# Performance work log

Measured on AMD Instinct MI355X. Metric: run time of the kernel, lower is better.

## Reference

```python
import jax, jax.numpy as jnp
import numpy as np

EPS = 1e-8      # F.normalize eps in _cos_angle
TOPK = 4
DELTA = 1.0     # huber delta
EXTRA_FRAMES = (1, 3, 5, 7)            # teacher-only frames
SHARED = ((2, 1), (4, 2), (6, 3))      # (teacher_idx, student_idx) for shared frames


def _huber(e):
    ae = jnp.abs(e)
    return jnp.where(ae <= DELTA, 0.5 * e * e, DELTA * (ae - 0.5 * DELTA))


def _angles(R, H, Sh):
    # R: [b,r,d] ref, H: [b,r,k,d] sim_high, Sh: [b,s,d] shared.
    # Cosines of the three triplet angles computed via dot-product expansion,
    # avoiding any [b,r,s,k,d] intermediate. cos = (u.v)/(max(|u|,eps)*max(|v|,eps))
    RH  = jnp.einsum('brd,brkd->brk', R, H)
    RSh = jnp.einsum('brd,bsd->brs', R, Sh)
    HSh = jnp.einsum('brkd,bsd->brsk', H, Sh)
    Rn2  = jnp.sum(R * R, -1)        # [b,r]
    Hn2  = jnp.sum(H * H, -1)        # [b,r,k]
    Shn2 = jnp.sum(Sh * Sh, -1)      # [b,s]
    n_RSh = jnp.maximum(jnp.sqrt(jnp.maximum(Rn2[:, :, None] + Shn2[:, None, :] - 2 * RSh, 0.0)), EPS)          # |R-Sh| [b,r,s]
    n_RH  = jnp.maximum(jnp.sqrt(jnp.maximum(Rn2[:, :, None] + Hn2 - 2 * RH, 0.0)), EPS)                        # |R-H|  [b,r,k]
    n_HSh = jnp.maximum(jnp.sqrt(jnp.maximum(Hn2[:, :, None, :] + Shn2[:, None, :, None] - 2 * HSh, 0.0)), EPS) # |H-Sh| [b,r,s,k]
    # angle1: vertex=ref, u=Sh-R, v=H-R
    d1 = HSh - RSh[..., None] - RH[:, :, None, :] + Rn2[:, :, None, None]
    a1 = d1 / (n_RSh[..., None] * n_RH[:, :, None, :])
    # angle2: vertex=H, u=R-H, v=Sh-H
    d2 = RSh[..., None] - RH[:, :, None, :] - HSh + Hn2[:, :, None, :]
    a2 = d2 / (n_RH[:, :, None, :] * n_HSh)
    # angle3: vertex=Sh, u=R-Sh, v=H-Sh
    d3 = RH[:, :, None, :] - RSh[..., None] - HSh + Shn2[:, None, :, None]
    a3 = d3 / (n_RSh[..., None] * n_HSh)
    return a1, a2, a3


def setup_inputs() -> dict:
    key = jax.random.key(0)
    k1, k2, k3, k4 = jax.random.split(key, 4)
    B, S_T, P, D = 2, 8, 2048, 1024
    num_ref, num_shared = 128, 128
    teacher_feats = jax.random.normal(k1, (B, S_T, P, D), jnp.float32)
    student_feats = jax.random.normal(k2, (B, 4, P, D), jnp.float32)
    ref_perm = jax.random.permutation(k3, P)[:num_ref].astype(jnp.int32)
    shared_perm = jax.random.permutation(k4, P)[:num_shared].astype(jnp.int32)
    return {"teacher_feats": teacher_feats, "student_feats": student_feats,
            "ref_perm": ref_perm, "shared_perm": shared_perm}


def reference(teacher_feats, student_feats, ref_perm, shared_perm):
    tf = jax.lax.stop_gradient(teacher_feats)  # teacher is fully detached
    B, _, P, D = tf.shape
    num_ref = ref_perm.shape[0]
    num_shared = shared_perm.shape[0]
    ref_t = tf[:, 0, ref_perm, :]                 # [B,R,D]
    ref_s = student_feats[:, 0, ref_perm, :]
    # teacher-only frames, concatenated along patch dim -> [B, EP, D]
    extra = tf[:, jnp.array(EXTRA_FRAMES), :, :].reshape(B, -1, D)
    # cosine-similarity retrieval (selection_mode='topk')
    rtn = ref_t / jnp.maximum(jnp.linalg.norm(ref_t, axis=-1, keepdims=True), 1e-12)
    etn = extra / jnp.maximum(jnp.linalg.norm(extra, axis=-1, keepdims=True), 1e-12)
    sim = jnp.einsum('brd,bed->bre', rtn, etn)
    _, idx = jax.lax.top_k(sim, TOPK)             # [B,R,K]
    H = jnp.take_along_axis(extra, idx.reshape(B, -1, 1), axis=1).reshape(B, num_ref, TOPK, D)
    s1 = s2 = s3 = jnp.float32(0.0)
    for tidx, sidx in SHARED:
        Sh_t = tf[:, tidx, shared_perm, :]
        Sh_s = student_feats[:, sidx, shared_perm, :]
        a1t, a2t, a3t = _angles(ref_t, H, Sh_t)
        a1s, a2s, a3s = _angles(ref_s, H, Sh_s)
        s1 = s1 + _huber(a1s - a1t).sum()
        s2 = s2 + _huber(a2s - a2t).sum()
        s3 = s3 + _huber(a3s - a3t).sum()
    total = jnp.float32(len(SHARED) * B * num_ref * num_shared * TOPK)
    # angle weights all 1.0
    loss = s1 / total + s2 / total + s3 / total
    return loss
```

## Files before the change

kernel.cpp:

```cpp
#include <hip/hip_runtime.h>
#include <cstdint>
#include <cstddef>
#include <cfloat>
#include <climits>

#define D_DIM   1024
#define P_DIM   2048
#define NB      2
#define NR      128
#define NS      128
#define KTOP    4
#define E_DIM   8192
#define ANG_EPS 1e-8f
#define M_PAIR  768
#define N_PAIR  768

#define SIM_SLICES  4
#define SIM_KSLICE  256
#define PAIR_SLICES 8
#define PAIR_KSLICE 128

#define TOPK_DELTA  0.25f
#define MAXCAND     128
#define LOSS_BLOCKS (NR * NB * 3)

typedef short short8 __attribute__((ext_vector_type(8)));
typedef float f32x4 __attribute__((ext_vector_type(4)));

__device__ __forceinline__ float dot4(float4 a, float4 b) {
  return a.x * b.x + a.y * b.y + a.z * b.z + a.w * b.w;
}

__device__ __forceinline__ float huber(float e) {
  float ae = fabsf(e);
  return ae <= 1.0f ? 0.5f * e * e : ae - 0.5f;
}

__device__ __forceinline__ bool better(float va, int ia, float vb, int ib) {
  return (va > vb) || (va == vb && ia < ib);
}

__device__ __forceinline__ unsigned int f2bf(float x) {
  union { float f; unsigned int u; } v; v.f = x;
  unsigned int r = v.u + 0x7fffu + ((v.u >> 16) & 1u);
  return r >> 16;
}
__device__ __forceinline__ unsigned int pk2bf(float x, float y) {
  return f2bf(x) | (f2bf(y) << 16);
}

__device__ __forceinline__ float block_reduce_sum(float v, float* scratch) {
  #pragma unroll
  for (int o = 32; o > 0; o >>= 1) v += __shfl_down(v, o);
  __syncthreads();
  if ((threadIdx.x & 63) == 0) scratch[threadIdx.x >> 6] = v;
  __syncthreads();
  float r = 0.0f;
  int nw = (int)(blockDim.x >> 6);
  if ((int)threadIdx.x < nw) r = scratch[threadIdx.x];
  #pragma unroll
  for (int o = 2; o > 0; o >>= 1) r += __shfl_down(r, o);
  return r;
}

__global__ __launch_bounds__(256) void sim_gemm_kernel(const float* __restrict__ tf,
                                                       const int* __restrict__ ref_perm,
                                                       float* __restrict__ simP,
                                                       float* __restrict__ bn2P) {
  __shared__ unsigned int Ah[128 * 20];
  __shared__ unsigned int Bh[128 * 20];
  __shared__ const float* Arow[128];
  __shared__ const float* Brow[128];
  const int tid = threadIdx.x;
  const int b = blockIdx.z;
  const int slice = blockIdx.y;
  const int nbase = blockIdx.x * 128;
  const int kbase = slice * SIM_KSLICE;
  if (tid < 128) {
    Arow[tid] = tf + ((size_t)(b * 8) * P_DIM + ref_perm[tid]) * D_DIM + kbase;
  } else {
    int n = nbase + (tid - 128);
    Brow[tid - 128] = tf + ((size_t)(b * 8 + 1 + 2 * (n >> 11)) * P_DIM + (n & (P_DIM - 1))) * D_DIM + kbase;
  }
  __syncthreads();

  const int srow = tid >> 1;
  const int shalf = (tid & 1) * 16;
  const float* asrc = Arow[srow] + shalf;
  const float* bsrc = Brow[srow] + shalf;

  float4 av[4], bv[4];
  #pragma unroll
  for (int i = 0; i < 4; ++i) {
    av[i] = *(const float4*)(asrc + 4 * i);
    bv[i] = *(const float4*)(bsrc + 4 * i);
  }

  const int wave = tid >> 6;
  const int lane = tid & 63;
  const int fr = lane & 15;
  const int q16 = (lane >> 4) * 16;
  const char* Ab = (const char*)Ah;
  const char* Bb = (const char*)Bh;

  f32x4 acc[2][8];
  #pragma unroll
  for (int mt = 0; mt < 2; ++mt)
    #pragma unroll
    for (int nt = 0; nt < 8; ++nt)
      #pragma unroll
      for (int r = 0; r < 4; ++r) acc[mt][nt][r] = 0.0f;

  float bn2 = 0.0f;
  unsigned int* adst = Ah + srow * 20 + (tid & 1) * 8;
  unsigned int* bdst = Bh + srow * 20 + (tid & 1) * 8;

  for (int ck = 0; ck < 8; ++ck) {
    bn2 += dot4(bv[0], bv[0]) + dot4(bv[1], bv[1]) + dot4(bv[2], bv[2]) + dot4(bv[3], bv[3]);
    unsigned int ua[8], ub[8];
    #pragma unroll
    for (int i = 0; i < 4; ++i) {
      ua[2 * i]     = pk2bf(av[i].x, av[i].y);
      ua[2 * i + 1] = pk2bf(av[i].z, av[i].w);
      ub[2 * i]     = pk2bf(bv[i].x, bv[i].y);
      ub[2 * i + 1] = pk2bf(bv[i].z, bv[i].w);
    }
    __syncthreads();
    *(uint4*)(adst)     = make_uint4(ua[0], ua[1], ua[2], ua[3]);
    *(uint4*)(adst + 4) = make_uint4(ua[4], ua[5], ua[6], ua[7]);
    *(uint4*)(bdst)     = make_uint4(ub[0], ub[1], ub[2], ub[3]);
    *(uint4*)(bdst + 4) = make_uint4(ub[4], ub[5], ub[6], ub[7]);
    __syncthreads();
    if (ck < 7) {
      const float* an = asrc + (ck + 1) * 32;
      const float* bn = bsrc + (ck + 1) * 32;
      #pragma unroll
      for (int i = 0; i < 4; ++i) {
        av[i] = *(const float4*)(an + 4 * i);
        bv[i] = *(const float4*)(bn + 4 * i);
      }
    }
    short8 afr[2], bfr[8];
    #pragma unroll
    for (int mt = 0; mt < 2; ++mt)
      afr[mt] = *(const short8*)(Ab + (wave * 32 + mt * 16 + fr) * 80 + q16);
    #pragma unroll
    for (int nt = 0; nt < 8; ++nt)
      bfr[nt] = *(const short8*)(Bb + (nt * 16 + fr) * 80 + q16);
    #pragma unroll
    for (int mt = 0; mt < 2; ++mt)
      #pragma unroll
      for (int nt = 0; nt < 8; ++nt)
        acc[mt][nt] = __builtin_amdgcn_mfma_f32_16x16x32_bf16(afr[mt], bfr[nt], acc[mt][nt], 0, 0, 0);
  }

  bn2 += __shfl_xor(bn2, 1);
  if ((tid & 1) == 0)
    bn2P[((size_t)slice * NB + b) * E_DIM + nbase + srow] = bn2;

  float* base = simP + (((size_t)slice * NB + b) * NR) * E_DIM + nbase;
  const int crow = (lane >> 4) * 4;
  #pragma unroll
  for (int mt = 0; mt < 2; ++mt) {
    #pragma unroll
    for (int nt = 0; nt < 8; ++nt) {
      int col = nt * 16 + fr;
      #pragma unroll
      for (int r = 0; r < 4; ++r) {
        int m = wave * 32 + mt * 16 + crow + r;
        base[(size_t)m * E_DIM + col] = acc[mt][nt][r];
      }
    }
  }
}

__global__ __launch_bounds__(256) void topk_kernel(const float* __restrict__ simP,
                                                   const float* __restrict__ bn2P,
                                                   const float* __restrict__ tf,
                                                   const float* __restrict__ sf,
                                                   const int* __restrict__ ref_perm,
                                                   int* __restrict__ tki,
                                                   float* __restrict__ rt_n2,
                                                   float* __restrict__ rs_n2,
                                                   float* __restrict__ hn2,
                                                   float* __restrict__ rh_t,
                                                   float* __restrict__ rh_s) {
  __shared__ float scores[E_DIM];
  __shared__ float sv[1024];
  __shared__ int si[1024];
  __shared__ float candVal[MAXCAND];
  __shared__ int candIdx[MAXCAND];
  __shared__ int cnt;
  __shared__ int fin4[4];
  const int tid = threadIdx.x;
  const int br = blockIdx.x;
  const int b = br >> 7;
  const int r = br & 127;
  const size_t ST = (size_t)NB * NR * E_DIM;
  const size_t SN = (size_t)NB * E_DIM;
  const float* p = simP + (size_t)br * E_DIM;
  const float* q = bn2P + (size_t)b * E_DIM;
  if (tid == 0) cnt = 0;

  float tv[4] = {-FLT_MAX, -FLT_MAX, -FLT_MAX, -FLT_MAX};
  int ti[4] = {INT_MAX, INT_MAX, INT_MAX, INT_MAX};
  for (int e4 = tid * 4; e4 < E_DIM; e4 += 1024) {
    float4 s = *(const float4*)(p + e4);
    float4 s1 = *(const float4*)(p + ST + e4);
    float4 s2 = *(const float4*)(p + 2 * ST + e4);
    float4 s3 = *(const float4*)(p + 3 * ST + e4);
    float4 n0 = *(const float4*)(q + e4);
    float4 n1 = *(const float4*)(q + SN + e4);
    float4 n2 = *(const float4*)(q + 2 * SN + e4);
    float4 n3 = *(const float4*)(q + 3 * SN + e4);
    float sj[4] = {s.x + s1.x + s2.x + s3.x, s.y + s1.y + s2.y + s3.y,
                   s.z + s1.z + s2.z + s3.z, s.w + s1.w + s2.w + s3.w};
    float nj[4] = {n0.x + n1.x + n2.x + n3.x, n0.y + n1.y + n2.y + n3.y,
                   n0.z + n1.z + n2.z + n3.z, n0.w + n1.w + n2.w + n3.w};
    #pragma unroll
    for (int j = 0; j < 4; ++j) {
      int e = e4 + j;
      float x = sj[j] * rsqrtf(fmaxf(nj[j], 1e-24f));
      scores[e] = x;
      if (better(x, e, tv[3], ti[3])) {
        tv[3] = x; ti[3] = e;
        #pragma unroll
        for (int k = 3; k > 0; --k) {
          if (better(tv[k], ti[k], tv[k - 1], ti[k - 1])) {
            float fv = tv[k]; tv[k] = tv[k - 1]; tv[k - 1] = fv;
            int fi2 = ti[k]; ti[k] = ti[k - 1]; ti[k - 1] = fi2;
          }
        }
      }
    }
  }
  #pragma unroll
  for (int k = 0; k < 4; ++k) { sv[tid * 4 + k] = tv[k]; si[tid * 4 + k] = ti[k]; }
  for (int stride = 128; stride > 0; stride >>= 1) {
    __syncthreads();
    if (tid < stride) {
      float av[4], bv2[4]; int ai[4], bi2[4];
      #pragma unroll
      for (int k = 0; k < 4; ++k) {
        av[k] = sv[tid * 4 + k];               ai[k] = si[tid * 4 + k];
        bv2[k] = sv[(tid + stride) * 4 + k];   bi2[k] = si[(tid + stride) * 4 + k];
      }
      float ov[4]; int oi[4]; int pa = 0, pb = 0;
      #pragma unroll
      for (int k = 0; k < 4; ++k) {
        bool takeA = (pa < 4) && (pb >= 4 || better(av[pa], ai[pa], bv2[pb], bi2[pb]));
        if (takeA) { ov[k] = av[pa]; oi[k] = ai[pa]; ++pa; }
        else       { ov[k] = bv2[pb]; oi[k] = bi2[pb]; ++pb; }
      }
      #pragma unroll
      for (int k = 0; k < 4; ++k) { sv[tid * 4 + k] = ov[k]; si[tid * 4 + k] = oi[k]; }
    }
  }
  __syncthreads();
  const float tau = sv[3] - TOPK_DELTA;

  for (int e4 = tid * 4; e4 < E_DIM; e4 += 1024) {
    #pragma unroll
    for (int j = 0; j < 4; ++j) {
      int e = e4 + j;
      if (scores[e] >= tau) {
        int pos = atomicAdd(&cnt, 1);
        if (pos < MAXCAND) candIdx[pos] = e;
      }
    }
  }
  __syncthreads();
  int cntc = min(cnt, MAXCAND);

  const float* R = tf + ((size_t)(b * 8) * P_DIM + ref_perm[r]) * D_DIM;
  const int wave = tid >> 6;
  const int lane = tid & 63;
  for (int c = wave; c < cntc; c += 4) {
    int e = candIdx[c];
    const float* E = tf + ((size_t)(b * 8 + 1 + 2 * (e >> 11)) * P_DIM + (e & (P_DIM - 1))) * D_DIM;
    float d = 0.0f, n2 = 0.0f;
    #pragma unroll
    for (int i = 0; i < 4; ++i) {
      float4 rv = *(const float4*)(R + lane * 16 + i * 4);
      float4 ev = *(const float4*)(E + lane * 16 + i * 4);
      d += dot4(rv, ev);
      n2 += dot4(ev, ev);
    }
    #pragma unroll
    for (int o = 32; o > 0; o >>= 1) { d += __shfl_xor(d, o); n2 += __shfl_xor(n2, o); }
    if (lane == 0) candVal[c] = d / fmaxf(sqrtf(n2), 1e-12f);
  }
  __syncthreads();
  if (tid == 0) {
    float bv[4] = {-FLT_MAX, -FLT_MAX, -FLT_MAX, -FLT_MAX};
    int bi[4] = {INT_MAX, INT_MAX, INT_MAX, INT_MAX};
    for (int c = 0; c < cntc; ++c) {
      float x = candVal[c]; int e = candIdx[c];
      if (better(x, e, bv[3], bi[3])) {
        bv[3] = x; bi[3] = e;
        #pragma unroll
        for (int k = 3; k > 0; --k) {
          if (better(bv[k], bi[k], bv[k - 1], bi[k - 1])) {
            float fv = bv[k]; bv[k] = bv[k - 1]; bv[k - 1] = fv;
            int fi2 = bi[k]; bi[k] = bi[k - 1]; bi[k - 1] = fi2;
          }
        }
      }
    }
    #pragma unroll
    for (int k = 0; k < 4; ++k) { tki[br * 4 + k] = bi[k]; fin4[k] = bi[k]; }
  }
  __syncthreads();

  {
    const float* RS = sf + ((size_t)(b * 4) * P_DIM + ref_perm[r]) * D_DIM;
    int e = fin4[wave];
    const float* H = tf + ((size_t)(b * 8 + 1 + 2 * (e >> 11)) * P_DIM + (e & (P_DIM - 1))) * D_DIM;
    float h2 = 0.0f, rht = 0.0f, rhs = 0.0f, rtn = 0.0f, rsn = 0.0f;
    #pragma unroll
    for (int i = 0; i < 4; ++i) {
      float4 rv = *(const float4*)(R + lane * 16 + i * 4);
      float4 sv2 = *(const float4*)(RS + lane * 16 + i * 4);
      float4 hv = *(const float4*)(H + lane * 16 + i * 4);
      h2 += dot4(hv, hv);
      rht += dot4(rv, hv);
      rhs += dot4(sv2, hv);
      rtn += dot4(rv, rv);
      rsn += dot4(sv2, sv2);
    }
    #pragma unroll
    for (int o = 32; o > 0; o >>= 1) {
      h2 += __shfl_xor(h2, o);
      rht += __shfl_xor(rht, o);
      rhs += __shfl_xor(rhs, o);
      rtn += __shfl_xor(rtn, o);
      rsn += __shfl_xor(rsn, o);
    }
    if (lane == 0) {
      hn2[br * KTOP + wave] = h2;
      rh_t[br * KTOP + wave] = rht;
      rh_s[br * KTOP + wave] = rhs;
      if (wave == 0) rt_n2[br] = rtn;
      if (wave == 1) rs_n2[br] = rsn;
    }
  }
}

__global__ __launch_bounds__(256) void pair_gemm_kernel(const float* __restrict__ tf,
                                                        const float* __restrict__ sf,
                                                        const int* __restrict__ ref_perm,
                                                        const int* __restrict__ shared_perm,
                                                        const int* __restrict__ tki,
                                                        float* __restrict__ CpP,
                                                        float* __restrict__ shb2P) {
  __shared__ unsigned int Ah[128 * 20];
  __shared__ unsigned int Bh[128 * 20];
  __shared__ const float* Arow[128];
  __shared__ const float* Brow[128];
  const int tid = threadIdx.x;
  const int b = blockIdx.z & 1;
  const int slice = blockIdx.z >> 1;
  const int mbase = blockIdx.y * 128;
  const int nbase = blockIdx.x * 128;
  const int kbase = slice * PAIR_KSLICE;
  if (tid < 128) {
    int m = mbase + tid;
    const float* p;
    if (m < 128) {
      p = tf + ((size_t)(b * 8) * P_DIM + ref_perm[m]) * D_DIM;
    } else if (m < 256) {
      p = sf + ((size_t)(b * 4) * P_DIM + ref_perm[m - 128]) * D_DIM;
    } else {
      int h = m - 256, r = h >> 2, k = h & 3;
      int e = tki[(b * NR + r) * KTOP + k];
      p = tf + ((size_t)(b * 8 + 1 + 2 * (e >> 11)) * P_DIM + (e & (P_DIM - 1))) * D_DIM;
    }
    Arow[tid] = p + kbase;
  } else {
    int n = nbase + (tid - 128);
    int pr = n >> 8, rem = n & 255, side = rem >> 7, s = rem & 127;
    const float* p;
    if (side == 0) p = tf + ((size_t)(b * 8 + 2 * pr + 2) * P_DIM + shared_perm[s]) * D_DIM;
    else           p = sf + ((size_t)(b * 4 + pr + 1) * P_DIM + shared_perm[s]) * D_DIM;
    Brow[tid - 128] = p + kbase;
  }
  __syncthreads();

  const int srow = tid >> 1;
  const int shalf = (tid & 1) * 16;
  const float* asrc = Arow[srow] + shalf;
  const float* bsrc = Brow[srow] + shalf;

  float4 av[4], bv[4];
  #pragma unroll
  for (int i = 0; i < 4; ++i) {
    av[i] = *(const float4*)(asrc + 4 * i);
    bv[i] = *(const float4*)(bsrc + 4 * i);
  }

  const int wave = tid >> 6;
  const int lane = tid & 63;
  const int fr = lane & 15;
  const int q16 = (lane >> 4) * 16;
  const char* Ab = (const char*)Ah;
  const char* Bb = (const char*)Bh;

  f32x4 acc[2][8];
  #pragma unroll
  for (int mt = 0; mt < 2; ++mt)
    #pragma unroll
    for (int nt = 0; nt < 8; ++nt)
      #pragma unroll
      for (int r = 0; r < 4; ++r) acc[mt][nt][r] = 0.0f;

  float bn2 = 0.0f;
  unsigned int* adst = Ah + srow * 20 + (tid & 1) * 8;
  unsigned int* bdst = Bh + srow * 20 + (tid & 1) * 8;

  for (int ck = 0; ck < 4; ++ck) {
    bn2 += dot4(bv[0], bv[0]) + dot4(bv[1], bv[1]) + dot4(bv[2], bv[2]) + dot4(bv[3], bv[3]);
    unsigned int ua[8], ub[8];
    #pragma unroll
    for (int i = 0; i < 4; ++i) {
      ua[2 * i]     = pk2bf(av[i].x, av[i].y);
      ua[2 * i + 1] = pk2bf(av[i].z, av[i].w);
      ub[2 * i]     = pk2bf(bv[i].x, bv[i].y);
      ub[2 * i + 1] = pk2bf(bv[i].z, bv[i].w);
    }
    __syncthreads();
    *(uint4*)(adst)     = make_uint4(ua[0], ua[1], ua[2], ua[3]);
    *(uint4*)(adst + 4) = make_uint4(ua[4], ua[5], ua[6], ua[7]);
    *(uint4*)(bdst)     = make_uint4(ub[0], ub[1], ub[2], ub[3]);
    *(uint4*)(bdst + 4) = make_uint4(ub[4], ub[5], ub[6], ub[7]);
    __syncthreads();
    if (ck < 3) {
      const float* an = asrc + (ck + 1) * 32;
      const float* bn = bsrc + (ck + 1) * 32;
      #pragma unroll
      for (int i = 0; i < 4; ++i) {
        av[i] = *(const float4*)(an + 4 * i);
        bv[i] = *(const float4*)(bn + 4 * i);
      }
    }
    short8 afr[2], bfr[8];
    #pragma unroll
    for (int mt = 0; mt < 2; ++mt)
      afr[mt] = *(const short8*)(Ab + (wave * 32 + mt * 16 + fr) * 80 + q16);
    #pragma unroll
    for (int nt = 0; nt < 8; ++nt)
      bfr[nt] = *(const short8*)(Bb + (nt * 16 + fr) * 80 + q16);
    #pragma unroll
    for (int mt = 0; mt < 2; ++mt)
      #pragma unroll
      for (int nt = 0; nt < 8; ++nt)
        acc[mt][nt] = __builtin_amdgcn_mfma_f32_16x16x32_bf16(afr[mt], bfr[nt], acc[mt][nt], 0, 0, 0);
  }

  bn2 += __shfl_xor(bn2, 1);
  if ((tid & 1) == 0)
    shb2P[((size_t)slice * NB + b) * N_PAIR + nbase + srow] = bn2;

  float* base = CpP + (((size_t)slice * NB + b) * M_PAIR + mbase) * N_PAIR + nbase;
  const int crow = (lane >> 4) * 4;
  #pragma unroll
  for (int mt = 0; mt < 2; ++mt) {
    #pragma unroll
    for (int nt = 0; nt < 8; ++nt) {
      int col = nt * 16 + fr;
      #pragma unroll
      for (int r = 0; r < 4; ++r) {
        int m = wave * 32 + mt * 16 + crow + r;
        base[(size_t)m * N_PAIR + col] = acc[mt][nt][r];
      }
    }
  }
}

__global__ __launch_bounds__(128) void loss_kernel(const float* __restrict__ CpP,
                                                   const float* __restrict__ rt_n2,
                                                   const float* __restrict__ rs_n2,
                                                   const float* __restrict__ hn2,
                                                   const float* __restrict__ rh_t,
                                                   const float* __restrict__ rh_s,
                                                   const float* __restrict__ shb2P,
                                                   float* __restrict__ acc,
                                                   float* __restrict__ out) {
  __shared__ float scr[2];
  int r = blockIdx.x, b = blockIdx.y, p = blockIdx.z;
  int s = threadIdx.x;
  int br = b * NR + r;
  const size_t SLC = (size_t)NB * M_PAIR * N_PAIR;
  const float* Cb = CpP + (size_t)b * M_PAIR * N_PAIR;
  auto sumC = [&](int m, int n) -> float {
    const float* q = Cb + (size_t)m * N_PAIR + n;
    float v = 0.0f;
    #pragma unroll
    for (int sl = 0; sl < PAIR_SLICES; ++sl) v += q[sl * SLC];
    return v;
  };
  float Rt2 = rt_n2[br], Rs2 = rs_n2[br];
  float St2 = 0.0f, Ss2 = 0.0f;
  {
    const float* qn = shb2P + (size_t)b * N_PAIR + p * 256 + s;
    #pragma unroll
    for (int sl = 0; sl < PAIR_SLICES; ++sl) {
      St2 += qn[(size_t)sl * NB * N_PAIR];
      Ss2 += qn[(size_t)sl * NB * N_PAIR + 128];
    }
  }
  float RSt = sumC(r, p * 256 + s);
  float RSs = sumC(128 + r, p * 256 + 128 + s);
  float sum = 0.0f;
  #pragma unroll
  for (int k = 0; k < KTOP; ++k) {
    float H2 = hn2[br * KTOP + k];
    float RHt = rh_t[br * KTOP + k];
    float RHs = rh_s[br * KTOP + k];
    float HSt = sumC(256 + r * 4 + k, p * 256 + s);
    float HSs = sumC(256 + r * 4 + k, p * 256 + 128 + s);
    float nRSt = fmaxf(sqrtf(fmaxf(Rt2 + St2 - 2.0f * RSt, 0.0f)), ANG_EPS);
    float nRHt = fmaxf(sqrtf(fmaxf(Rt2 + H2 - 2.0f * RHt, 0.0f)), ANG_EPS);
    float nHSt = fmaxf(sqrtf(fmaxf(H2 + St2 - 2.0f * HSt, 0.0f)), ANG_EPS);
    float a1t = (HSt - RSt - RHt + Rt2) / (nRSt * nRHt);
    float a2t = (RSt - RHt - HSt + H2) / (nRHt * nHSt);
    float a3t = (RHt - RSt - HSt + St2) / (nRSt * nHSt);
    float nRSs = fmaxf(sqrtf(fmaxf(Rs2 + Ss2 - 2.0f * RSs, 0.0f)), ANG_EPS);
    float nRHs = fmaxf(sqrtf(fmaxf(Rs2 + H2 - 2.0f * RHs, 0.0f)), ANG_EPS);
    float nHSs = fmaxf(sqrtf(fmaxf(H2 + Ss2 - 2.0f * HSs, 0.0f)), ANG_EPS);
    float a1s = (HSs - RSs - RHs + Rs2) / (nRSs * nRHs);
    float a2s = (RSs - RHs - HSs + H2) / (nRHs * nHSs);
    float a3s = (RHs - RSs - HSs + Ss2) / (nRSs * nHSs);
    sum += huber(a1s - a1t) + huber(a2s - a2t) + huber(a3s - a3t);
  }
  float tot = block_reduce_sum(sum, scr);
  if (threadIdx.x == 0) {
    atomicAdd(acc, tot);
    __threadfence();
    int done = atomicAdd((int*)(acc + 1), 1);
    if (done == LOSS_BLOCKS - 1) {
      float total = atomicAdd(acc, 0.0f);
      out[0] = total * (1.0f / 393216.0f);
    }
  }
}

extern "C" void kernel_launch(void* const* d_in, const int* in_sizes, int n_in,
                              void* d_out, int out_size, void* d_ws, size_t ws_size,
                              hipStream_t stream) {
  const float* tf = (const float*)d_in[0];
  const float* sf = (const float*)d_in[1];
  const int* ref_perm = (const int*)d_in[2];
  const int* shared_perm = (const int*)d_in[3];
  float* ws = (float*)d_ws;

  float* simP   = ws;
  float* bn2P   = simP + (size_t)SIM_SLICES * NB * NR * E_DIM;
  float* CpP    = bn2P + (size_t)SIM_SLICES * NB * E_DIM;
  float* shb2P  = CpP  + (size_t)PAIR_SLICES * NB * M_PAIR * N_PAIR;
  float* rt_n2  = shb2P + (size_t)PAIR_SLICES * NB * N_PAIR;
  float* rs_n2  = rt_n2  + NB * NR;
  float* hn2    = rs_n2  + NB * NR;
  float* rh_t   = hn2    + NB * NR * KTOP;
  float* rh_s   = rh_t   + NB * NR * KTOP;
  float* acc    = rh_s   + NB * NR * KTOP;
  int*   tki    = (int*)(acc + 4);
  float* out = (float*)d_out;

  hipMemsetAsync(acc, 0, 2 * sizeof(float), stream);
  sim_gemm_kernel<<<dim3(E_DIM / 128, SIM_SLICES, NB), 256, 0, stream>>>(tf, ref_perm, simP, bn2P);
  topk_kernel<<<NB * NR, 256, 0, stream>>>(simP, bn2P, tf, sf, ref_perm, tki,
                                           rt_n2, rs_n2, hn2, rh_t, rh_s);
  pair_gemm_kernel<<<dim3(N_PAIR / 128, M_PAIR / 128, NB * PAIR_SLICES), 256, 0, stream>>>(
      tf, sf, ref_perm, shared_perm, tki, CpP, shb2P);
  loss_kernel<<<dim3(NR, NB, 3), 128, 0, stream>>>(CpP, rt_n2, rs_n2, hn2, rh_t, rh_s,
                                                   shb2P, acc, out);
}
```

Measured before the change: 293.6 us.

## Fuse per-tile top-k selection into similarity GEMM and drop split-K partials

The similarity GEMM no longer splits K into slices. Each block now computes the full dot products, normalizes them by column norms, and extracts a per-row local top-8 candidate list into a small pool. This replaces writing and re-reading a large partial similarity matrix (4 slices × 2×128×8192 floats). A lighter merge kernel then reduces the 64 local lists per row and selects the threshold candidates from the pooled entries. In exchange, the sim kernel launches only 128 blocks with a serial per-row scan, which lowers parallelism. Separately, the pair GEMM drops from 8 to 4 K-slices, giving more work per block and fewer partials to write.

```diff
diff --git a/kernel.cpp b/kernel.cpp
--- a/kernel.cpp
+++ b/kernel.cpp
@@ -15,13 +15,15 @@
 #define M_PAIR  768
 #define N_PAIR  768
 
-#define SIM_SLICES  4
-#define SIM_KSLICE  256
-#define PAIR_SLICES 8
-#define PAIR_KSLICE 128
+#define SIM_CHUNKS  32
+#define SIM_NBLK    64
+#define PAIR_SLICES 4
+#define PAIR_KSLICE 256
+#define PAIR_CHUNKS 8
 
 #define TOPK_DELTA  0.25f
-#define MAXCAND     128
+#define NLOC        8
+#define MAXCAND     64
 #define LOSS_BLOCKS (NR * NB * 3)
 
 typedef short short8 __attribute__((ext_vector_type(8)));
@@ -65,22 +67,21 @@
 
 __global__ __launch_bounds__(256) void sim_gemm_kernel(const float* __restrict__ tf,
                                                        const int* __restrict__ ref_perm,
-                                                       float* __restrict__ simP,
-                                                       float* __restrict__ bn2P) {
+                                                       float2* __restrict__ pool) {
   __shared__ unsigned int Ah[128 * 20];
   __shared__ unsigned int Bh[128 * 20];
   __shared__ const float* Arow[128];
   __shared__ const float* Brow[128];
+  __shared__ float scores[128][133];
+  __shared__ float coln2[128];
   const int tid = threadIdx.x;
-  const int b = blockIdx.z;
-  const int slice = blockIdx.y;
+  const int b = blockIdx.y;
   const int nbase = blockIdx.x * 128;
-  const int kbase = slice * SIM_KSLICE;
   if (tid < 128) {
-    Arow[tid] = tf + ((size_t)(b * 8) * P_DIM + ref_perm[tid]) * D_DIM + kbase;
+    Arow[tid] = tf + ((size_t)(b * 8) * P_DIM + ref_perm[tid]) * D_DIM;
   } else {
     int n = nbase + (tid - 128);
-    Brow[tid - 128] = tf + ((size_t)(b * 8 + 1 + 2 * (n >> 11)) * P_DIM + (n & (P_DIM - 1))) * D_DIM + kbase;
+    Brow[tid - 128] = tf + ((size_t)(b * 8 + 1 + 2 * (n >> 11)) * P_DIM + (n & (P_DIM - 1))) * D_DIM;
   }
   __syncthreads();
 
@@ -115,7 +116,7 @@
   unsigned int* adst = Ah + srow * 20 + (tid & 1) * 8;
   unsigned int* bdst = Bh + srow * 20 + (tid & 1) * 8;
 
-  for (int ck = 0; ck < 8; ++ck) {
+  for (int ck = 0; ck < SIM_CHUNKS; ++ck) {
     bn2 += dot4(bv[0], bv[0]) + dot4(bv[1], bv[1]) + dot4(bv[2], bv[2]) + dot4(bv[3], bv[3]);
     unsigned int ua[8], ub[8];
     #pragma unroll
@@ -131,7 +132,7 @@
     *(uint4*)(bdst)     = make_uint4(ub[0], ub[1], ub[2], ub[3]);
     *(uint4*)(bdst + 4) = make_uint4(ub[4], ub[5], ub[6], ub[7]);
     __syncthreads();
-    if (ck < 7) {
+    if (ck < SIM_CHUNKS - 1) {
       const float* an = asrc + (ck + 1) * 32;
       const float* bn = bsrc + (ck + 1) * 32;
       #pragma unroll
@@ -155,37 +156,60 @@
   }
 
   bn2 += __shfl_xor(bn2, 1);
-  if ((tid & 1) == 0)
-    bn2P[((size_t)slice * NB + b) * E_DIM + nbase + srow] = bn2;
-
-  float* base = simP + (((size_t)slice * NB + b) * NR) * E_DIM + nbase;
+  if ((tid & 1) == 0) coln2[srow] = bn2;
+  __syncthreads();
+
   const int crow = (lane >> 4) * 4;
   #pragma unroll
   for (int mt = 0; mt < 2; ++mt) {
     #pragma unroll
     for (int nt = 0; nt < 8; ++nt) {
       int col = nt * 16 + fr;
+      float inv = rsqrtf(fmaxf(coln2[col], 1e-24f));
       #pragma unroll
       for (int r = 0; r < 4; ++r) {
         int m = wave * 32 + mt * 16 + crow + r;
-        base[(size_t)m * E_DIM + col] = acc[mt][nt][r];
-      }
-    }
-  }
-}
-
-__global__ __launch_bounds__(256) void topk_kernel(const float* __restrict__ simP,
-                                                   const float* __restrict__ bn2P,
-                                                   const float* __restrict__ tf,
-                                                   const float* __restrict__ sf,
-                                                   const int* __restrict__ ref_perm,
-                                                   int* __restrict__ tki,
-                                                   float* __restrict__ rt_n2,
-                                                   float* __restrict__ rs_n2,
-                                                   float* __restrict__ hn2,
-                                                   float* __restrict__ rh_t,
-                                                   float* __restrict__ rh_s) {
-  __shared__ float scores[E_DIM];
+        scores[m][col] = acc[mt][nt][r] * inv;
+      }
+    }
+  }
+  __syncthreads();
+
+  if (tid < 128) {
+    float tv[NLOC]; int ti[NLOC];
+    #pragma unroll
+    for (int k = 0; k < NLOC; ++k) { tv[k] = -FLT_MAX; ti[k] = INT_MAX; }
+    for (int col = 0; col < 128; ++col) {
+      float x = scores[tid][col];
+      int e = nbase + col;
+      if (better(x, e, tv[NLOC - 1], ti[NLOC - 1])) {
+        tv[NLOC - 1] = x; ti[NLOC - 1] = e;
+        #pragma unroll
+        for (int k = NLOC - 1; k > 0; --k) {
+          if (better(tv[k], ti[k], tv[k - 1], ti[k - 1])) {
+            float fv = tv[k]; tv[k] = tv[k - 1]; tv[k - 1] = fv;
+            int fi2 = ti[k]; ti[k] = ti[k - 1]; ti[k - 1] = fi2;
+          }
+        }
+      }
+    }
+    float2* dst = pool + (((size_t)(b * NR + tid)) * SIM_NBLK + blockIdx.x) * NLOC;
+    #pragma unroll
+    for (int k = 0; k < NLOC; ++k)
+      dst[k] = make_float2(tv[k], __int_as_float(ti[k]));
+  }
+}
+
+__global__ __launch_bounds__(256) void topk_merge_kernel(const float2* __restrict__ pool,
+                                                         const float* __restrict__ tf,
+                                                         const float* __restrict__ sf,
+                                                         const int* __restrict__ ref_perm,
+                                                         int* __restrict__ tki,
+                                                         float* __restrict__ rt_n2,
+                                                         float* __restrict__ rs_n2,
+                                                         float* __restrict__ hn2,
+                                                         float* __restrict__ rh_t,
+                                                         float* __restrict__ rh_s) {
   __shared__ float sv[1024];
   __shared__ int si[1024];
   __shared__ float candVal[MAXCAND];
@@ -196,46 +220,20 @@
   const int br = blockIdx.x;
   const int b = br >> 7;
   const int r = br & 127;
-  const size_t ST = (size_t)NB * NR * E_DIM;
-  const size_t SN = (size_t)NB * E_DIM;
-  const float* p = simP + (size_t)br * E_DIM;
-  const float* q = bn2P + (size_t)b * E_DIM;
   if (tid == 0) cnt = 0;
 
-  float tv[4] = {-FLT_MAX, -FLT_MAX, -FLT_MAX, -FLT_MAX};
-  int ti[4] = {INT_MAX, INT_MAX, INT_MAX, INT_MAX};
-  for (int e4 = tid * 4; e4 < E_DIM; e4 += 1024) {
-    float4 s = *(const float4*)(p + e4);
-    float4 s1 = *(const float4*)(p + ST + e4);
-    float4 s2 = *(const float4*)(p + 2 * ST + e4);
-    float4 s3 = *(const float4*)(p + 3 * ST + e4);
-    float4 n0 = *(const float4*)(q + e4);
-    float4 n1 = *(const float4*)(q + SN + e4);
-    float4 n2 = *(const float4*)(q + 2 * SN + e4);
-    float4 n3 = *(const float4*)(q + 3 * SN + e4);
-    float sj[4] = {s.x + s1.x + s2.x + s3.x, s.y + s1.y + s2.y + s3.y,
-                   s.z + s1.z + s2.z + s3.z, s.w + s1.w + s2.w + s3.w};
-    float nj[4] = {n0.x + n1.x + n2.x + n3.x, n0.y + n1.y + n2.y + n3.y,
-                   n0.z + n1.z + n2.z + n3.z, n0.w + n1.w + n2.w + n3.w};
-    #pragma unroll
-    for (int j = 0; j < 4; ++j) {
-      int e = e4 + j;
-      float x = sj[j] * rsqrtf(fmaxf(nj[j], 1e-24f));
-      scores[e] = x;
-      if (better(x, e, tv[3], ti[3])) {
-        tv[3] = x; ti[3] = e;
-        #pragma unroll
-        for (int k = 3; k > 0; --k) {
-          if (better(tv[k], ti[k], tv[k - 1], ti[k - 1])) {
-            float fv = tv[k]; tv[k] = tv[k - 1]; tv[k - 1] = fv;
-            int fi2 = ti[k]; ti[k] = ti[k - 1]; ti[k - 1] = fi2;
-          }
-        }
-      }
-    }
-  }
-  #pragma unroll
-  for (int k = 0; k < 4; ++k) { sv[tid * 4 + k] = tv[k]; si[tid * 4 + k] = ti[k]; }
+  const float2* pp = pool + (size_t)br * (SIM_NBLK * NLOC);
+  float2 e0 = pp[tid * 2];
+  float2 e1 = pp[tid * 2 + 1];
+  float v0 = e0.x, v1 = e1.x;
+  int i0 = __float_as_int(e0.y), i1 = __float_as_int(e1.y);
+
+  float lv[4]; int li[4];
+  if (better(v0, i0, v1, i1)) { lv[0] = v0; li[0] = i0; lv[1] = v1; li[1] = i1; }
+  else                        { lv[0] = v1; li[0] = i1; lv[1] = v0; li[1] = i0; }
+  lv[2] = lv[3] = -FLT_MAX; li[2] = li[3] = INT_MAX;
+  #pragma unroll
+  for (int k = 0; k < 4; ++k) { sv[tid * 4 + k] = lv[k]; si[tid * 4 + k] = li[k]; }
   for (int stride = 128; stride > 0; stride >>= 1) {
     __syncthreads();
     if (tid < stride) {
@@ -259,16 +257,8 @@
   __syncthreads();
   const float tau = sv[3] - TOPK_DELTA;
 
-  for (int e4 = tid * 4; e4 < E_DIM; e4 += 1024) {
-    #pragma unroll
-    for (int j = 0; j < 4; ++j) {
-      int e = e4 + j;
-      if (scores[e] >= tau) {
-        int pos = atomicAdd(&cnt, 1);
-        if (pos < MAXCAND) candIdx[pos] = e;
-      }
-    }
-  }
+  if (v0 >= tau) { int pos = atomicAdd(&cnt, 1); if (pos < MAXCAND) candIdx[pos] = i0; }
+  if (v1 >= tau) { int pos = atomicAdd(&cnt, 1); if (pos < MAXCAND) candIdx[pos] = i1; }
   __syncthreads();
   int cntc = min(cnt, MAXCAND);
 
@@ -417,7 +407,7 @@
   unsigned int* adst = Ah + srow * 20 + (tid & 1) * 8;
   unsigned int* bdst = Bh + srow * 20 + (tid & 1) * 8;
 
-  for (int ck = 0; ck < 4; ++ck) {
+  for (int ck = 0; ck < PAIR_CHUNKS; ++ck) {
     bn2 += dot4(bv[0], bv[0]) + dot4(bv[1], bv[1]) + dot4(bv[2], bv[2]) + dot4(bv[3], bv[3]);
     unsigned int ua[8], ub[8];
     #pragma unroll
@@ -433,7 +423,7 @@
     *(uint4*)(bdst)     = make_uint4(ub[0], ub[1], ub[2], ub[3]);
     *(uint4*)(bdst + 4) = make_uint4(ub[4], ub[5], ub[6], ub[7]);
     __syncthreads();
-    if (ck < 3) {
+    if (ck < PAIR_CHUNKS - 1) {
       const float* an = asrc + (ck + 1) * 32;
       const float* bn = bsrc + (ck + 1) * 32;
       #pragma unroll
@@ -553,9 +543,8 @@
   const int* shared_perm = (const int*)d_in[3];
   float* ws = (float*)d_ws;
 
-  float* simP   = ws;
-  float* bn2P   = simP + (size_t)SIM_SLICES * NB * NR * E_DIM;
-  float* CpP    = bn2P + (size_t)SIM_SLICES * NB * E_DIM;
+  float2* pool  = (float2*)ws;
+  float* CpP    = ws + (size_t)2 * NB * NR * SIM_NBLK * NLOC;
   float* shb2P  = CpP  + (size_t)PAIR_SLICES * NB * M_PAIR * N_PAIR;
   float* rt_n2  = shb2P + (size_t)PAIR_SLICES * NB * N_PAIR;
   float* rs_n2  = rt_n2  + NB * NR;
@@ -567,9 +556,9 @@
   float* out = (float*)d_out;
 
   hipMemsetAsync(acc, 0, 2 * sizeof(float), stream);
-  sim_gemm_kernel<<<dim3(E_DIM / 128, SIM_SLICES, NB), 256, 0, stream>>>(tf, ref_perm, simP, bn2P);
-  topk_kernel<<<NB * NR, 256, 0, stream>>>(simP, bn2P, tf, sf, ref_perm, tki,
-                                           rt_n2, rs_n2, hn2, rh_t, rh_s);
+  sim_gemm_kernel<<<dim3(SIM_NBLK, NB), 256, 0, stream>>>(tf, ref_perm, pool);
+  topk_merge_kernel<<<NB * NR, 256, 0, stream>>>(pool, tf, sf, ref_perm, tki,
+                                                 rt_n2, rs_n2, hn2, rh_t, rh_s);
   pair_gemm_kernel<<<dim3(N_PAIR / 128, M_PAIR / 128, NB * PAIR_SLICES), 256, 0, stream>>>(
       tf, sf, ref_perm, shared_perm, tki, CpP, shb2P);
   loss_kernel<<<dim3(NR, NB, 3), 128, 0, stream>>>(CpP, rt_n2, rs_n2, hn2, rh_t, rh_s,
```

Measured after the change: 380.1 us. 29.4% more time.
